# Optimization experiments

Hardware: AMD Instinct MI355X
Metric: run time of the kernel (lower is better)

## Reference

```python
import jax, jax.numpy as jnp
import numpy as np

B, S, D = 4, 2048, 1024
E = 8            # num_experts
H = 2 * D        # int(4*D*(1/top_k)) with top_k=2, scaling_factor='auto'


def setup_inputs() -> dict:
    key = jax.random.key(0)
    ks = jax.random.split(key, 8)
    sd = 1.0 / np.sqrt(D)
    sh = 1.0 / np.sqrt(H)
    return {
        "x": jax.random.normal(ks[0], (B, S, D), dtype=jnp.float32),
        "top_k": 2,
        "Wg": jax.random.uniform(ks[1], (D, E), jnp.float32, -sd, sd),
        "bg": jax.random.uniform(ks[2], (E,), jnp.float32, -sd, sd),
        "W1": jax.random.uniform(ks[3], (E, D, H), jnp.float32, -sd, sd),
        "b1": jax.random.uniform(ks[4], (E, H), jnp.float32, -sd, sd),
        "W2": jax.random.uniform(ks[5], (E, H, D), jnp.float32, -sh, sh),
        "b2": jax.random.uniform(ks[6], (E, D), jnp.float32, -sh, sh),
    }


def reference(x, top_k, Wg, bg, W1, b1, W2, b2):
    b, s, d = x.shape
    e = W1.shape[0]
    T = b * s
    xt = x.reshape(T, d)                                   # [T, D]
    gate_logits = xt @ Wg + bg                             # [T, E]
    gate_probas = jax.nn.softmax(gate_logits, axis=-1)
    topk_p, topk_i = jax.lax.top_k(gate_probas, top_k)     # [T, K]
    topk_p = topk_p / jnp.sum(topk_p, axis=-1, keepdims=True)
    # combine weights per expert: zero for unselected experts
    w = jnp.zeros((T, e), dtype=x.dtype).at[jnp.arange(T)[:, None], topk_i].add(topk_p)  # [T, E]
    # dense grouped FFN over experts; unselected experts are zero-weighted,
    # so the weighted combine matches the original gather-MLP-scatter math
    h = jax.nn.gelu(jnp.einsum('td,edh->teh', xt, W1) + b1, approximate=True)  # [T, E, H]
    y = jnp.einsum('teh,ehd->ted', h, W2) + b2             # [T, E, D]
    out = jnp.einsum('te,ted->td', w, y)                   # [T, D]
    return out.reshape(b, s, d)
```

## Files before the change

kernel.cpp:

```cpp
#include <hip/hip_runtime.h>

typedef unsigned short u16;
typedef short v8s __attribute__((ext_vector_type(8)));
typedef float v4f __attribute__((ext_vector_type(4)));

constexpr int Tn = 8192;
constexpr int Dd = 1024;
constexpr int Hh = 2048;
constexpr int Ee = 8;
constexpr int NB = 32;

static __device__ __forceinline__ u16 f2bf(float v) {
  unsigned u = __float_as_uint(v);
  unsigned r = (u + 0x7fffu + ((u >> 16) & 1u)) >> 16;
  return (u16)r;
}

static __device__ __forceinline__ float bf2f(u16 v) {
  return __uint_as_float(((unsigned)v) << 16);
}

static __device__ __forceinline__ void gload_lds16(const u16* g, u16* l) {
  __builtin_amdgcn_global_load_lds(
      (const __attribute__((address_space(1))) unsigned int*)g,
      (__attribute__((address_space(3))) unsigned int*)l, 16, 0, 0);
}

__global__ void convert_x_kernel(const float* __restrict__ x, u16* __restrict__ xb) {
  size_t i = ((size_t)blockIdx.x * 256 + threadIdx.x) * 4;
  float4 v = *reinterpret_cast<const float4*>(x + i);
  ushort4 o;
  o.x = f2bf(v.x); o.y = f2bf(v.y); o.z = f2bf(v.z); o.w = f2bf(v.w);
  *reinterpret_cast<ushort4*>(xb + i) = o;
}

__global__ void transpose_cvt_kernel(const float* __restrict__ in, u16* __restrict__ out,
                                     int R, int C) {
  __shared__ float tile[32][33];
  int e = blockIdx.z;
  const float* ip = in + (size_t)e * R * C;
  u16* op = out + (size_t)e * R * C;
  int c0 = blockIdx.x * 32, r0 = blockIdx.y * 32;
  int tx = threadIdx.x, ty = threadIdx.y;
  for (int i = ty; i < 32; i += 8)
    tile[i][tx] = ip[(size_t)(r0 + i) * C + c0 + tx];
  __syncthreads();
  for (int i = ty; i < 32; i += 8)
    op[(size_t)(c0 + i) * R + r0 + tx] = f2bf(tile[tx][i]);
}

__global__ __launch_bounds__(256) void gating_kernel(
    const float* __restrict__ x, const float* __restrict__ Wg, const float* __restrict__ bg,
    int* __restrict__ topki, float* __restrict__ topkw) {
  int lane = threadIdx.x & 63;
  int t = blockIdx.x * 4 + (threadIdx.x >> 6);
  const float4* xr = reinterpret_cast<const float4*>(x + (size_t)t * Dd);
  float acc[8] = {0.f, 0.f, 0.f, 0.f, 0.f, 0.f, 0.f, 0.f};
#pragma unroll
  for (int it = 0; it < 4; ++it) {
    float4 xv = xr[it * 64 + lane];
    int r = it * 256 + lane * 4;
    const float4* wr = reinterpret_cast<const float4*>(Wg + (size_t)r * 8);
    float xs[4] = {xv.x, xv.y, xv.z, xv.w};
#pragma unroll
    for (int q = 0; q < 4; ++q) {
      float4 a = wr[q * 2], b = wr[q * 2 + 1];
      acc[0] += xs[q] * a.x; acc[1] += xs[q] * a.y; acc[2] += xs[q] * a.z; acc[3] += xs[q] * a.w;
      acc[4] += xs[q] * b.x; acc[5] += xs[q] * b.y; acc[6] += xs[q] * b.z; acc[7] += xs[q] * b.w;
    }
  }
#pragma unroll
  for (int e = 0; e < 8; ++e) {
#pragma unroll
    for (int off = 32; off > 0; off >>= 1) acc[e] += __shfl_xor(acc[e], off, 64);
  }
  if (lane == 0) {
    float l[8];
    float mx = -1e30f;
#pragma unroll
    for (int e = 0; e < 8; ++e) { l[e] = acc[e] + bg[e]; mx = fmaxf(mx, l[e]); }
    int i0 = 0;
#pragma unroll
    for (int e = 1; e < 8; ++e) if (l[e] > l[i0]) i0 = e;
    int i1 = (i0 == 0) ? 1 : 0;
#pragma unroll
    for (int e = 0; e < 8; ++e) if (e != i0 && l[e] > l[i1]) i1 = e;
    float e0 = __expf(l[i0] - mx), e1 = __expf(l[i1] - mx);
    float inv = 1.0f / (e0 + e1);
    topki[2 * t] = i0; topki[2 * t + 1] = i1;
    topkw[2 * t] = e0 * inv; topkw[2 * t + 1] = e1 * inv;
  }
}

__global__ __launch_bounds__(256) void hist_kernel(const int* __restrict__ topki,
                                                   int* __restrict__ blockcnt) {
  __shared__ int bins[8];
  int tid = threadIdx.x, b = blockIdx.x;
  if (tid < 8) bins[tid] = 0;
  __syncthreads();
  atomicAdd(&bins[topki[b * 512 + tid]], 1);
  atomicAdd(&bins[topki[b * 512 + 256 + tid]], 1);
  __syncthreads();
  if (tid < 8) blockcnt[b * 8 + tid] = bins[tid];
}

__global__ void prefix_kernel(const int* __restrict__ blockcnt, int* __restrict__ offs,
                              int* __restrict__ blockstart) {
  __shared__ int tmp[8][NB];
  __shared__ int tot[8];
  int tid = threadIdx.x;
  if (tid < 8) {
    int s = 0;
    for (int b = 0; b < NB; ++b) { tmp[tid][b] = s; s += blockcnt[b * 8 + tid]; }
    tot[tid] = s;
  }
  __syncthreads();
  if (tid == 0) {
    int o = 0;
    for (int e = 0; e < 8; ++e) { offs[e] = o; o += tot[e]; }
    offs[8] = o;
  }
  __syncthreads();
  if (tid < 8)
    for (int b = 0; b < NB; ++b) blockstart[b * 8 + tid] = offs[tid] + tmp[tid][b];
}

__global__ __launch_bounds__(256) void scatter_kernel(
    const int* __restrict__ topki, const int* __restrict__ blockstart,
    int* __restrict__ rows, int* __restrict__ slotmap) {
  __shared__ int lbins[8];
  int tid = threadIdx.x, b = blockIdx.x;
  if (tid < 8) lbins[tid] = blockstart[b * 8 + tid];
  __syncthreads();
#pragma unroll
  for (int j = 0; j < 2; ++j) {
    int idx = b * 512 + j * 256 + tid;
    int e = topki[idx];
    int slot = atomicAdd(&lbins[e], 1);
    rows[slot] = idx >> 1;
    slotmap[idx] = slot;
  }
}

__global__ __launch_bounds__(256, 2) void gemm1_kernel(
    const u16* __restrict__ xb, const u16* __restrict__ w1t, const float* __restrict__ b1,
    const int* __restrict__ offs, const int* __restrict__ rows, u16* __restrict__ hbuf) {
  const int e = blockIdx.z;
  const int base = offs[e];
  const int cnt = offs[e + 1] - base;
  const int m0 = blockIdx.y * 128;
  if (m0 >= cnt) return;
  const int n0 = blockIdx.x * 128;

  __shared__ u16 As[128 * 32];
  __shared__ u16 Bs[128 * 32];

  const int tid = threadIdx.x;
  const int lane = tid & 63;
  const int wid = tid >> 6;
  const int wm = (wid >> 1) * 64;
  const int wn = (wid & 1) * 64;
  const int l16 = lane & 15;
  const int quad = lane >> 4;

  const u16* aga[2];
  const u16* bga[2];
  u16* alds[2];
  u16* blds[2];
#pragma unroll
  for (int j = 0; j < 2; ++j) {
    int chunk = wid * 2 + j;
    int row = chunk * 16 + (lane >> 2);
    int kcol = (lane & 3) * 8;
    int ar = (m0 + row < cnt) ? (m0 + row) : 0;
    aga[j] = xb + (size_t)rows[base + ar] * Dd + kcol;
    bga[j] = w1t + ((size_t)e * Hh + n0 + row) * Dd + kcol;
    alds[j] = As + chunk * 512;
    blds[j] = Bs + chunk * 512;
  }

  v4f acc[4][4];
#pragma unroll
  for (int i = 0; i < 4; ++i)
#pragma unroll
    for (int j = 0; j < 4; ++j) acc[i][j] = {0.f, 0.f, 0.f, 0.f};

  for (int k0 = 0; k0 < Dd; k0 += 32) {
    __syncthreads();
    gload_lds16(aga[0] + k0, alds[0]);
    gload_lds16(aga[1] + k0, alds[1]);
    gload_lds16(bga[0] + k0, blds[0]);
    gload_lds16(bga[1] + k0, blds[1]);
    __syncthreads();

    v8s a[4], b[4];
#pragma unroll
    for (int mt = 0; mt < 4; ++mt)
      a[mt] = *reinterpret_cast<const v8s*>(&As[(wm + mt * 16 + l16) * 32 + quad * 8]);
#pragma unroll
    for (int nt = 0; nt < 4; ++nt)
      b[nt] = *reinterpret_cast<const v8s*>(&Bs[(wn + nt * 16 + l16) * 32 + quad * 8]);
#pragma unroll
    for (int mt = 0; mt < 4; ++mt)
#pragma unroll
      for (int nt = 0; nt < 4; ++nt)
        acc[mt][nt] = __builtin_amdgcn_mfma_f32_16x16x32_bf16(a[mt], b[nt], acc[mt][nt], 0, 0, 0);
  }

  float b1v[4];
  int ng[4];
#pragma unroll
  for (int nt = 0; nt < 4; ++nt) {
    ng[nt] = n0 + wn + nt * 16 + l16;
    b1v[nt] = b1[(size_t)e * Hh + ng[nt]];
  }
#pragma unroll
  for (int mt = 0; mt < 4; ++mt) {
#pragma unroll
    for (int i = 0; i < 4; ++i) {
      int m = wm + mt * 16 + quad * 4 + i;
      if (m0 + m < cnt) {
        size_t rowbase = (size_t)(base + m0 + m) * Hh;
#pragma unroll
        for (int nt = 0; nt < 4; ++nt) {
          float v = acc[mt][nt][i] + b1v[nt];
          float g = 0.5f * v * (1.0f + tanhf(0.7978845608028654f * (v + 0.044715f * v * v * v)));
          hbuf[rowbase + ng[nt]] = f2bf(g);
        }
      }
    }
  }
}

__global__ __launch_bounds__(256, 2) void gemm2_kernel(
    const u16* __restrict__ hbuf, const u16* __restrict__ w2t, const float* __restrict__ b2,
    const int* __restrict__ offs, u16* __restrict__ ybuf) {
  const int e = blockIdx.z;
  const int base = offs[e];
  const int cnt = offs[e + 1] - base;
  const int m0 = blockIdx.y * 128;
  if (m0 >= cnt) return;
  const int n0 = blockIdx.x * 128;

  __shared__ u16 As[128 * 32];
  __shared__ u16 Bs[128 * 32];

  const int tid = threadIdx.x;
  const int lane = tid & 63;
  const int wid = tid >> 6;
  const int wm = (wid >> 1) * 64;
  const int wn = (wid & 1) * 64;
  const int l16 = lane & 15;
  const int quad = lane >> 4;

  const u16* aga[2];
  const u16* bga[2];
  u16* alds[2];
  u16* blds[2];
#pragma unroll
  for (int j = 0; j < 2; ++j) {
    int chunk = wid * 2 + j;
    int row = chunk * 16 + (lane >> 2);
    int kcol = (lane & 3) * 8;
    int ar = (m0 + row < cnt) ? (m0 + row) : 0;
    aga[j] = hbuf + (size_t)(base + ar) * Hh + kcol;
    bga[j] = w2t + ((size_t)e * Dd + n0 + row) * Hh + kcol;
    alds[j] = As + chunk * 512;
    blds[j] = Bs + chunk * 512;
  }

  v4f acc[4][4];
#pragma unroll
  for (int i = 0; i < 4; ++i)
#pragma unroll
    for (int j = 0; j < 4; ++j) acc[i][j] = {0.f, 0.f, 0.f, 0.f};

  for (int k0 = 0; k0 < Hh; k0 += 32) {
    __syncthreads();
    gload_lds16(aga[0] + k0, alds[0]);
    gload_lds16(aga[1] + k0, alds[1]);
    gload_lds16(bga[0] + k0, blds[0]);
    gload_lds16(bga[1] + k0, blds[1]);
    __syncthreads();

    v8s a[4], b[4];
#pragma unroll
    for (int mt = 0; mt < 4; ++mt)
      a[mt] = *reinterpret_cast<const v8s*>(&As[(wm + mt * 16 + l16) * 32 + quad * 8]);
#pragma unroll
    for (int nt = 0; nt < 4; ++nt)
      b[nt] = *reinterpret_cast<const v8s*>(&Bs[(wn + nt * 16 + l16) * 32 + quad * 8]);
#pragma unroll
    for (int mt = 0; mt < 4; ++mt)
#pragma unroll
      for (int nt = 0; nt < 4; ++nt)
        acc[mt][nt] = __builtin_amdgcn_mfma_f32_16x16x32_bf16(a[mt], b[nt], acc[mt][nt], 0, 0, 0);
  }

  float b2v[4];
  int ng[4];
#pragma unroll
  for (int nt = 0; nt < 4; ++nt) {
    ng[nt] = n0 + wn + nt * 16 + l16;
    b2v[nt] = b2[(size_t)e * Dd + ng[nt]];
  }
#pragma unroll
  for (int mt = 0; mt < 4; ++mt) {
#pragma unroll
    for (int i = 0; i < 4; ++i) {
      int m = wm + mt * 16 + quad * 4 + i;
      if (m0 + m < cnt) {
        size_t rowbase = (size_t)(base + m0 + m) * Dd;
#pragma unroll
        for (int nt = 0; nt < 4; ++nt)
          ybuf[rowbase + ng[nt]] = f2bf(acc[mt][nt][i] + b2v[nt]);
      }
    }
  }
}

__global__ __launch_bounds__(256) void combine_kernel(
    const u16* __restrict__ ybuf, const int* __restrict__ slotmap,
    const float* __restrict__ topkw, float* __restrict__ out) {
  int idx = blockIdx.x * 256 + threadIdx.x;
  int t = idx >> 7;
  int d0 = (idx & 127) * 8;
  int s0 = slotmap[2 * t], s1 = slotmap[2 * t + 1];
  float w0 = topkw[2 * t], w1 = topkw[2 * t + 1];
  uint4 ya = *reinterpret_cast<const uint4*>(ybuf + (size_t)s0 * Dd + d0);
  uint4 yb = *reinterpret_cast<const uint4*>(ybuf + (size_t)s1 * Dd + d0);
  float r[8];
  const unsigned* pa = &ya.x;
  const unsigned* pb = &yb.x;
#pragma unroll
  for (int j = 0; j < 4; ++j) {
    unsigned a = pa[j], b = pb[j];
    r[2 * j]     = w0 * bf2f((u16)(a & 0xffff)) + w1 * bf2f((u16)(b & 0xffff));
    r[2 * j + 1] = w0 * bf2f((u16)(a >> 16))    + w1 * bf2f((u16)(b >> 16));
  }
  float4* op = reinterpret_cast<float4*>(out + (size_t)t * Dd + d0);
  op[0] = make_float4(r[0], r[1], r[2], r[3]);
  op[1] = make_float4(r[4], r[5], r[6], r[7]);
}

extern "C" void kernel_launch(void* const* d_in, const int* in_sizes, int n_in,
                              void* d_out, int out_size, void* d_ws, size_t ws_size,
                              hipStream_t stream) {
  const float* x  = (const float*)d_in[0];
  const float* Wg = (const float*)d_in[2];
  const float* bg = (const float*)d_in[3];
  const float* W1 = (const float*)d_in[4];
  const float* b1 = (const float*)d_in[5];
  const float* W2 = (const float*)d_in[6];
  const float* b2 = (const float*)d_in[7];
  float* out = (float*)d_out;

  char* p = (char*)d_ws;
  auto take = [&](size_t bytes) {
    char* q = p;
    p += (bytes + 255) & ~(size_t)255;
    return q;
  };
  int*   offs       = (int*)take(64);
  int*   blockcnt   = (int*)take((size_t)NB * 8 * sizeof(int));
  int*   blockstart = (int*)take((size_t)NB * 8 * sizeof(int));
  int*   topki      = (int*)take((size_t)Tn * 2 * sizeof(int));
  float* topkw      = (float*)take((size_t)Tn * 2 * sizeof(float));
  int*   rows       = (int*)take((size_t)Tn * 2 * sizeof(int));
  int*   slotmap    = (int*)take((size_t)Tn * 2 * sizeof(int));
  u16*   xb         = (u16*)take((size_t)Tn * Dd * 2);
  u16*   w1t        = (u16*)take((size_t)Ee * Dd * Hh * 2);
  u16*   w2t        = (u16*)take((size_t)Ee * Dd * Hh * 2);
  u16*   hbuf       = (u16*)take((size_t)Tn * 2 * Hh * 2);
  u16*   ybuf       = (u16*)take((size_t)Tn * 2 * Dd * 2);

  convert_x_kernel<<<(Tn * Dd) / 1024, 256, 0, stream>>>(x, xb);
  transpose_cvt_kernel<<<dim3(Hh / 32, Dd / 32, Ee), dim3(32, 8), 0, stream>>>(W1, w1t, Dd, Hh);
  transpose_cvt_kernel<<<dim3(Dd / 32, Hh / 32, Ee), dim3(32, 8), 0, stream>>>(W2, w2t, Hh, Dd);
  gating_kernel<<<Tn / 4, 256, 0, stream>>>(x, Wg, bg, topki, topkw);
  hist_kernel<<<NB, 256, 0, stream>>>(topki, blockcnt);
  prefix_kernel<<<1, 64, 0, stream>>>(blockcnt, offs, blockstart);
  scatter_kernel<<<NB, 256, 0, stream>>>(topki, blockstart, rows, slotmap);
  gemm1_kernel<<<dim3(Hh / 128, 64, Ee), 256, 0, stream>>>(xb, w1t, b1, offs, rows, hbuf);
  gemm2_kernel<<<dim3(Dd / 128, 64, Ee), 256, 0, stream>>>(hbuf, w2t, b2, offs, ybuf);
  combine_kernel<<<(Tn * Dd / 8) / 256, 256, 0, stream>>>(ybuf, slotmap, topkw, out);
}
```

Before: 498.7 us.

## Schedule GEMMs over a compact panel list with XCD-aware block mapping

The prefix kernel now builds a compact list of (expert, row-start) 128-row panels. Both grouped GEMMs launch a 1-D grid sized to the maximum possible panel count instead of a mostly-empty 3-D grid. The block index is mapped so that all N-tiles of one panel land on the same XCD, which is meant to improve L2 reuse of the A rows. Three smaller changes ride along: the x-to-bf16 conversion is folded into the gating kernel to drop a launch and a reread of x, the weight transposes use 64x64 tiles, and tanh-GELU is rewritten as an equivalent sigmoid form using fast __expf. The fast exp may slightly change numerics.

```diff
diff --git a/kernel.cpp b/kernel.cpp
--- a/kernel.cpp
+++ b/kernel.cpp
@@ -9,6 +9,7 @@
 constexpr int Hh = 2048;
 constexpr int Ee = 8;
 constexpr int NB = 32;
+constexpr int MAXP = 17;
 
 static __device__ __forceinline__ u16 f2bf(float v) {
   unsigned u = __float_as_uint(v);
@@ -26,32 +27,24 @@
       (__attribute__((address_space(3))) unsigned int*)l, 16, 0, 0);
 }
 
-__global__ void convert_x_kernel(const float* __restrict__ x, u16* __restrict__ xb) {
-  size_t i = ((size_t)blockIdx.x * 256 + threadIdx.x) * 4;
-  float4 v = *reinterpret_cast<const float4*>(x + i);
-  ushort4 o;
-  o.x = f2bf(v.x); o.y = f2bf(v.y); o.z = f2bf(v.z); o.w = f2bf(v.w);
-  *reinterpret_cast<ushort4*>(xb + i) = o;
-}
-
-__global__ void transpose_cvt_kernel(const float* __restrict__ in, u16* __restrict__ out,
-                                     int R, int C) {
-  __shared__ float tile[32][33];
+__global__ __launch_bounds__(512) void transpose_cvt_kernel(
+    const float* __restrict__ in, u16* __restrict__ out, int R, int C) {
+  __shared__ float tile[64][65];
   int e = blockIdx.z;
   const float* ip = in + (size_t)e * R * C;
   u16* op = out + (size_t)e * R * C;
-  int c0 = blockIdx.x * 32, r0 = blockIdx.y * 32;
+  int c0 = blockIdx.x * 64, r0 = blockIdx.y * 64;
   int tx = threadIdx.x, ty = threadIdx.y;
-  for (int i = ty; i < 32; i += 8)
+  for (int i = ty; i < 64; i += 8)
     tile[i][tx] = ip[(size_t)(r0 + i) * C + c0 + tx];
   __syncthreads();
-  for (int i = ty; i < 32; i += 8)
+  for (int i = ty; i < 64; i += 8)
     op[(size_t)(c0 + i) * R + r0 + tx] = f2bf(tile[tx][i]);
 }
 
 __global__ __launch_bounds__(256) void gating_kernel(
     const float* __restrict__ x, const float* __restrict__ Wg, const float* __restrict__ bg,
-    int* __restrict__ topki, float* __restrict__ topkw) {
+    int* __restrict__ topki, float* __restrict__ topkw, u16* __restrict__ xb) {
   int lane = threadIdx.x & 63;
   int t = blockIdx.x * 4 + (threadIdx.x >> 6);
   const float4* xr = reinterpret_cast<const float4*>(x + (size_t)t * Dd);
@@ -60,6 +53,9 @@
   for (int it = 0; it < 4; ++it) {
     float4 xv = xr[it * 64 + lane];
     int r = it * 256 + lane * 4;
+    ushort4 o;
+    o.x = f2bf(xv.x); o.y = f2bf(xv.y); o.z = f2bf(xv.z); o.w = f2bf(xv.w);
+    *reinterpret_cast<ushort4*>(xb + (size_t)t * Dd + r) = o;
     const float4* wr = reinterpret_cast<const float4*>(Wg + (size_t)r * 8);
     float xs[4] = {xv.x, xv.y, xv.z, xv.w};
 #pragma unroll
@@ -105,7 +101,9 @@
 }
 
 __global__ void prefix_kernel(const int* __restrict__ blockcnt, int* __restrict__ offs,
-                              int* __restrict__ blockstart) {
+                              int* __restrict__ blockstart,
+                              int* __restrict__ panelE, int* __restrict__ panelB,
+                              int* __restrict__ nPanels) {
   __shared__ int tmp[8][NB];
   __shared__ int tot[8];
   int tid = threadIdx.x;
@@ -119,6 +117,15 @@
     int o = 0;
     for (int e = 0; e < 8; ++e) { offs[e] = o; o += tot[e]; }
     offs[8] = o;
+    int np = 0;
+    for (int e = 0; e < 8; ++e) {
+      for (int m0 = 0; m0 < tot[e]; m0 += 128) {
+        panelE[np] = e;
+        panelB[np] = offs[e] + m0;
+        ++np;
+      }
+    }
+    *nPanels = np;
   }
   __syncthreads();
   if (tid < 8)
@@ -144,13 +151,19 @@
 
 __global__ __launch_bounds__(256, 2) void gemm1_kernel(
     const u16* __restrict__ xb, const u16* __restrict__ w1t, const float* __restrict__ b1,
-    const int* __restrict__ offs, const int* __restrict__ rows, u16* __restrict__ hbuf) {
-  const int e = blockIdx.z;
-  const int base = offs[e];
-  const int cnt = offs[e + 1] - base;
-  const int m0 = blockIdx.y * 128;
-  if (m0 >= cnt) return;
-  const int n0 = blockIdx.x * 128;
+    const int* __restrict__ offs, const int* __restrict__ rows,
+    const int* __restrict__ panelE, const int* __restrict__ panelB,
+    const int* __restrict__ nPanels, u16* __restrict__ hbuf) {
+  const int bid = blockIdx.x;
+  const int xcd = bid & 7;
+  const int q = bid >> 3;
+  const int n = q & 15;
+  const int pi = (q >> 4) * 8 + xcd;
+  if (pi >= *nPanels) return;
+  const int e = panelE[pi];
+  const int sbase = panelB[pi];
+  const int lim = offs[e + 1];
+  const int n0 = n * 128;
 
   __shared__ u16 As[128 * 32];
   __shared__ u16 Bs[128 * 32];
@@ -172,8 +185,9 @@
     int chunk = wid * 2 + j;
     int row = chunk * 16 + (lane >> 2);
     int kcol = (lane & 3) * 8;
-    int ar = (m0 + row < cnt) ? (m0 + row) : 0;
-    aga[j] = xb + (size_t)rows[base + ar] * Dd + kcol;
+    int slot = sbase + row;
+    if (slot >= lim) slot = sbase;
+    aga[j] = xb + (size_t)rows[slot] * Dd + kcol;
     bga[j] = w1t + ((size_t)e * Hh + n0 + row) * Dd + kcol;
     alds[j] = As + chunk * 512;
     blds[j] = Bs + chunk * 512;
@@ -219,13 +233,13 @@
 #pragma unroll
     for (int i = 0; i < 4; ++i) {
       int m = wm + mt * 16 + quad * 4 + i;
-      if (m0 + m < cnt) {
-        size_t rowbase = (size_t)(base + m0 + m) * Hh;
+      if (sbase + m < lim) {
+        size_t rowbase = (size_t)(sbase + m) * Hh;
 #pragma unroll
         for (int nt = 0; nt < 4; ++nt) {
           float v = acc[mt][nt][i] + b1v[nt];
-          float g = 0.5f * v * (1.0f + tanhf(0.7978845608028654f * (v + 0.044715f * v * v * v)));
-          hbuf[rowbase + ng[nt]] = f2bf(g);
+          float s = 1.0f / (1.0f + __expf(-1.5957691216057308f * (v + 0.044715f * v * v * v)));
+          hbuf[rowbase + ng[nt]] = f2bf(v * s);
         }
       }
     }
@@ -234,13 +248,19 @@
 
 __global__ __launch_bounds__(256, 2) void gemm2_kernel(
     const u16* __restrict__ hbuf, const u16* __restrict__ w2t, const float* __restrict__ b2,
-    const int* __restrict__ offs, u16* __restrict__ ybuf) {
-  const int e = blockIdx.z;
-  const int base = offs[e];
-  const int cnt = offs[e + 1] - base;
-  const int m0 = blockIdx.y * 128;
-  if (m0 >= cnt) return;
-  const int n0 = blockIdx.x * 128;
+    const int* __restrict__ offs,
+    const int* __restrict__ panelE, const int* __restrict__ panelB,
+    const int* __restrict__ nPanels, u16* __restrict__ ybuf) {
+  const int bid = blockIdx.x;
+  const int xcd = bid & 7;
+  const int q = bid >> 3;
+  const int n = q & 7;
+  const int pi = (q >> 3) * 8 + xcd;
+  if (pi >= *nPanels) return;
+  const int e = panelE[pi];
+  const int sbase = panelB[pi];
+  const int lim = offs[e + 1];
+  const int n0 = n * 128;
 
   __shared__ u16 As[128 * 32];
   __shared__ u16 Bs[128 * 32];
@@ -262,8 +282,9 @@
     int chunk = wid * 2 + j;
     int row = chunk * 16 + (lane >> 2);
     int kcol = (lane & 3) * 8;
-    int ar = (m0 + row < cnt) ? (m0 + row) : 0;
-    aga[j] = hbuf + (size_t)(base + ar) * Hh + kcol;
+    int slot = sbase + row;
+    if (slot >= lim) slot = sbase;
+    aga[j] = hbuf + (size_t)slot * Hh + kcol;
     bga[j] = w2t + ((size_t)e * Dd + n0 + row) * Hh + kcol;
     alds[j] = As + chunk * 512;
     blds[j] = Bs + chunk * 512;
@@ -309,8 +330,8 @@
 #pragma unroll
     for (int i = 0; i < 4; ++i) {
       int m = wm + mt * 16 + quad * 4 + i;
-      if (m0 + m < cnt) {
-        size_t rowbase = (size_t)(base + m0 + m) * Dd;
+      if (sbase + m < lim) {
+        size_t rowbase = (size_t)(sbase + m) * Dd;
 #pragma unroll
         for (int nt = 0; nt < 4; ++nt)
           ybuf[rowbase + ng[nt]] = f2bf(acc[mt][nt][i] + b2v[nt]);
@@ -364,6 +385,9 @@
   int*   offs       = (int*)take(64);
   int*   blockcnt   = (int*)take((size_t)NB * 8 * sizeof(int));
   int*   blockstart = (int*)take((size_t)NB * 8 * sizeof(int));
+  int*   panelE     = (int*)take(1024);
+  int*   panelB     = (int*)take(1024);
+  int*   nPanels    = (int*)take(256);
   int*   topki      = (int*)take((size_t)Tn * 2 * sizeof(int));
   float* topkw      = (float*)take((size_t)Tn * 2 * sizeof(float));
   int*   rows       = (int*)take((size_t)Tn * 2 * sizeof(int));
@@ -374,14 +398,15 @@
   u16*   hbuf       = (u16*)take((size_t)Tn * 2 * Hh * 2);
   u16*   ybuf       = (u16*)take((size_t)Tn * 2 * Dd * 2);
 
-  convert_x_kernel<<<(Tn * Dd) / 1024, 256, 0, stream>>>(x, xb);
-  transpose_cvt_kernel<<<dim3(Hh / 32, Dd / 32, Ee), dim3(32, 8), 0, stream>>>(W1, w1t, Dd, Hh);
-  transpose_cvt_kernel<<<dim3(Dd / 32, Hh / 32, Ee), dim3(32, 8), 0, stream>>>(W2, w2t, Hh, Dd);
-  gating_kernel<<<Tn / 4, 256, 0, stream>>>(x, Wg, bg, topki, topkw);
+  transpose_cvt_kernel<<<dim3(Hh / 64, Dd / 64, Ee), dim3(64, 8), 0, stream>>>(W1, w1t, Dd, Hh);
+  transpose_cvt_kernel<<<dim3(Dd / 64, Hh / 64, Ee), dim3(64, 8), 0, stream>>>(W2, w2t, Hh, Dd);
+  gating_kernel<<<Tn / 4, 256, 0, stream>>>(x, Wg, bg, topki, topkw, xb);
   hist_kernel<<<NB, 256, 0, stream>>>(topki, blockcnt);
-  prefix_kernel<<<1, 64, 0, stream>>>(blockcnt, offs, blockstart);
+  prefix_kernel<<<1, 64, 0, stream>>>(blockcnt, offs, blockstart, panelE, panelB, nPanels);
   scatter_kernel<<<NB, 256, 0, stream>>>(topki, blockstart, rows, slotmap);
-  gemm1_kernel<<<dim3(Hh / 128, 64, Ee), 256, 0, stream>>>(xb, w1t, b1, offs, rows, hbuf);
-  gemm2_kernel<<<dim3(Dd / 128, 64, Ee), 256, 0, stream>>>(hbuf, w2t, b2, offs, ybuf);
+  gemm1_kernel<<<8 * 16 * MAXP, 256, 0, stream>>>(xb, w1t, b1, offs, rows,
+                                                  panelE, panelB, nPanels, hbuf);
+  gemm2_kernel<<<8 * 8 * MAXP, 256, 0, stream>>>(hbuf, w2t, b2, offs,
+                                                 panelE, panelB, nPanels, ybuf);
   combine_kernel<<<(Tn * Dd / 8) / 256, 256, 0, stream>>>(ybuf, slotmap, topkw, out);
 }
```

Result: faster. 475.2 us (-4.7%).
